# Kernel optimization log

Hardware: AMD Instinct MI355X
Metric: run time of the kernel (lower is better)

Reference implementation:

```python
import jax, jax.numpy as jnp
import numpy as np

# ---- static config (matches init_kwargs) ----
B, SX, SY, SZ = 1, 64, 64, 64
W = 32            # HIDDEN_DIM
L = 4             # num_fourier_layers
M1 = M2 = M3 = 8  # fourier modes per axis
PX = PY = PZ = 8  # domain padding
ALPHA = 0.05      # leaky relu slope
OUTC = 6


def conv3d(x, w, pad):
    # x: (B,C,D,H,W), w: (O,I,kd,kh,kw)
    return jax.lax.conv_general_dilated(
        x, w, window_strides=(1, 1, 1), padding=[(pad, pad)] * 3,
        dimension_numbers=('NCDHW', 'OIDHW', 'NCDHW'))


def pad1(x):
    # periodic=(0,0,0) -> zero pad 1 on every spatial side (matches ZeroPad3d chain)
    return jnp.pad(x, ((0, 0), (0, 0), (1, 1), (1, 1), (1, 1)))


def basic_block(x, w1, w2):
    # BasicBlock3D_Periodic with use_shortcut=False
    out = jax.nn.leaky_relu(conv3d(pad1(x), w1, 0), ALPHA)
    return conv3d(pad1(out), w2, 0)


def spec_apply(xft_slice, w):
    # xft_slice: complex (B,C,d1,d2,d3); w: (2C,2C,5,5,5)
    re_im = jnp.concatenate([xft_slice.real, xft_slice.imag], axis=1)  # (B,2C,...)
    out = conv3d(re_im, w, 2)                                          # (B,2C,...)
    b, c2, d1, d2, d3 = out.shape
    out = out.reshape(b, c2 // 2, 2, d1, d2, d3)
    return jax.lax.complex(out[:, :, 0], out[:, :, 1])


def spectral_conv(x, ws):
    # ws: (8, 2W, 2W, 5, 5, 5); mode-limited per-octant conv in frequency space
    b, c, n, m, l = x.shape
    xft = jnp.fft.rfftn(x, axes=(-3, -2, -1))  # (b,c,n,m,l//2+1) complex
    out = jnp.zeros((b, c, n, m, l // 2 + 1), dtype=xft.dtype)
    octs = [
        (slice(None, M1),  slice(None, M2)),
        (slice(n - M1, None), slice(None, M2)),
        (slice(None, M1),  slice(m - M2, None)),
        (slice(n - M1, None), slice(m - M2, None)),
        (slice(M1, n - M1), slice(None, M2)),
        (slice(None, M1),  slice(M2, m - M2)),
        (slice(M1, n - M1), slice(m - M2, None)),
        (slice(n - M1, None), slice(M2, m - M2)),
    ]
    for i, (s1, s2) in enumerate(octs):
        out = out.at[:, :, s1, s2, :M3].set(spec_apply(xft[:, :, s1, s2, :M3], ws[i]))
    return jnp.fft.irfftn(out, s=(n, m, l), axes=(-3, -2, -1))


def setup_inputs() -> dict:
    key = jax.random.key(0)
    ks = jax.random.split(key, 16)
    f32 = jnp.float32
    d = {
        'yeex': jax.random.normal(ks[0], (B, SX, SY, SZ), f32),
        'yeey': jax.random.normal(ks[1], (B, SX, SY, SZ), f32),
        'yeez': jax.random.normal(ks[2], (B, SX, SY, SZ), f32),
        'fc0_w': jax.random.normal(ks[3], (6, W), f32) * 0.1,
        'fc0_b': jax.random.normal(ks[4], (W,), f32) * 0.01,
        'spec_w': jax.random.normal(ks[5], (L, 8, 2 * W, 2 * W, 5, 5, 5), f32) * 0.02,
        'blk_w1': jax.random.normal(ks[6], (L, W, W, 3, 3, 3), f32) * 0.05,
        'blk_w2': jax.random.normal(ks[7], (L, W, W, 3, 3, 3), f32) * 0.05,
        'fc1_w': jax.random.normal(ks[8], (W, 128), f32) * 0.05,
        'fc1_b': jax.random.normal(ks[9], (128,), f32) * 0.01,
        'fc2_w': jax.random.normal(ks[10], (128, OUTC), f32) * 0.05,
        'fc2_b': jax.random.normal(ks[11], (OUTC,), f32) * 0.01,
    }
    return d


def reference(yeex, yeey, yeez, fc0_w, fc0_b, spec_w, blk_w1, blk_w2,
              fc1_w, fc1_b, fc2_w, fc2_b):
    b, sx, sy, sz = yeez.shape
    # normalized coordinate grid (3 channels), as in standard FNO get_grid
    gx = jnp.broadcast_to(jnp.linspace(0., 1., sx, dtype=yeex.dtype)[None, :, None, None], (b, sx, sy, sz))
    gy = jnp.broadcast_to(jnp.linspace(0., 1., sy, dtype=yeex.dtype)[None, None, :, None], (b, sx, sy, sz))
    gz = jnp.broadcast_to(jnp.linspace(0., 1., sz, dtype=yeex.dtype)[None, None, None, :], (b, sx, sy, sz))
    inp = jnp.stack([yeex, yeey, yeez, gx, gy, gz], axis=-1)  # (b,sx,sy,sz,6)

    x = inp @ fc0_w + fc0_b                      # lift: (b,sx,sy,sz,W)
    x = jnp.transpose(x, (0, 4, 1, 2, 3))        # (b,W,sx,sy,sz)
    x = jnp.pad(x, ((0, 0), (0, 0), (0, PX), (0, PY), (0, PZ)))

    for i in range(L):
        x1 = spectral_conv(x, spec_w[i])
        x2 = basic_block(x, blk_w1[i], blk_w2[i])
        x = x1 + x2 + x
        if i < L - 1:
            x = jax.nn.leaky_relu(x, ALPHA)

    x = x[:, :, :sx, :sy, :sz]                   # crop domain padding
    x = jnp.transpose(x, (0, 2, 3, 4, 1))        # (b,sx,sy,sz,W)
    x = jax.nn.leaky_relu(x @ fc1_w + fc1_b, ALPHA)
    return x @ fc2_w + fc2_b                     # (b,sx,sy,sz,OUTC)
```

## Files before the change

### kernel.cpp

```cpp
#include <hip/hip_runtime.h>
#include <math.h>

#define NS 72
#define NS2 (NS*NS)
#define NS3 (NS*NS*NS)
#define MZ 8
#define LALPHA 0.05f
#define CSCALE (1.0f/256.0f)

typedef _Float16 f16x8 __attribute__((ext_vector_type(8)));
typedef _Float16 f16x4 __attribute__((ext_vector_type(4)));
typedef float f32x4 __attribute__((ext_vector_type(4)));

__device__ __forceinline__ float leakyf(float v){ return v > 0.f ? v : LALPHA*v; }

__constant__ int c_RX0[8] = {0,64,0,64, 8,0,8,64};
__constant__ int c_RNX[8] = {8,8,8,8, 56,8,56,8};
__constant__ int c_RY0[8] = {0,0,64,64, 0,8,64,8};
__constant__ int c_RNY[8] = {8,8,8,8, 8,56,8,56};
__constant__ int c_Bbase[8] = {0,1728,3456,5184, 6912,15552,24192,32832};
__constant__ int c_BY[8]    = {12,12,12,12, 12,60,12,60};

__global__ void k_tw(float2* tw){
  int t = threadIdx.x;
  if (t < NS){
    double th = (2.0*M_PI/72.0)*(double)t;
    tw[t] = make_float2((float)cos(th), (float)sin(th));
  }
}

__global__ void k_wpackT(const float* __restrict__ w1, float* __restrict__ w1t){
  int e = blockIdx.x*256 + threadIdx.x;
  int j = e >> 5, c = e & 31;
  w1t[e] = w1[c*128 + j];
}

__global__ void k_fc0(const float* __restrict__ yx, const float* __restrict__ yy,
                      const float* __restrict__ yz, const float* __restrict__ w,
                      const float* __restrict__ b, float* __restrict__ X){
  int idx = blockIdx.x*256 + threadIdx.x;
  int z = idx % NS; int t = idx / NS; int y = t % NS; t /= NS; int x = t % NS; int c = t / NS;
  float v = 0.f;
  if (x < 64 && y < 64 && z < 64){
    int p = (x*64 + y)*64 + z;
    float i0 = yx[p], i1 = yy[p], i2 = yz[p];
    float gx = (float)x*(1.f/63.f), gy = (float)y*(1.f/63.f), gz = (float)z*(1.f/63.f);
    v = b[c] + i0*w[0*32+c] + i1*w[1*32+c] + i2*w[2*32+c]
             + gx*w[3*32+c] + gy*w[4*32+c] + gz*w[5*32+c];
  }
  X[idx] = v;
}

__global__ void k_zdft(const float* __restrict__ X, float2* __restrict__ A, const float2* __restrict__ tw){
  __shared__ float2 stw[NS];
  int tid = threadIdx.x;
  if (tid < NS) stw[tid] = tw[tid];
  __syncthreads();
  int f = blockIdx.x*256 + tid;
  const float* row = X + (size_t)f*NS;
  float ar[MZ], ai[MZ]; int tk[MZ];
  #pragma unroll
  for (int k=0;k<MZ;k++){ ar[k]=0.f; ai[k]=0.f; tk[k]=0; }
  for (int z4=0; z4<NS; z4+=4){
    float4 v4 = *(const float4*)(row + z4);
    float vs[4] = {v4.x, v4.y, v4.z, v4.w};
    #pragma unroll
    for (int zz=0; zz<4; zz++){
      float v = vs[zz];
      #pragma unroll
      for (int k=0;k<MZ;k++){
        float2 w = stw[tk[k]];
        ar[k] += v*w.x;
        ai[k] -= v*w.y;
        tk[k] += k; if (tk[k] >= NS) tk[k] -= NS;
      }
    }
  }
  float2* o = A + (size_t)f*MZ;
  #pragma unroll
  for (int k=0;k<MZ;k++) o[k] = make_float2(ar[k], ai[k]);
}

__global__ void k_ydft(const float2* __restrict__ A, float2* __restrict__ B, const float2* __restrict__ tw){
  __shared__ float2 stw[NS];
  int tid = threadIdx.x;
  if (tid < NS) stw[tid] = tw[tid];
  __syncthreads();
  int f = blockIdx.x*256 + tid;
  int ky = f % NS; int cx = f / NS;
  const float2* in = A + (size_t)cx*NS*MZ;
  float ar[MZ], ai[MZ];
  #pragma unroll
  for (int k=0;k<MZ;k++){ ar[k]=0.f; ai[k]=0.f; }
  int t = 0;
  for (int y=0;y<NS;y++){
    float2 w = stw[t]; t += ky; if (t>=NS) t-=NS;
    const float2* iy = in + y*MZ;
    #pragma unroll
    for (int k=0;k<MZ;k++){
      float2 v = iy[k];
      ar[k] += v.x*w.x + v.y*w.y;
      ai[k] += v.y*w.x - v.x*w.y;
    }
  }
  float2* o = B + (size_t)f*MZ;
  #pragma unroll
  for (int k=0;k<MZ;k++) o[k] = make_float2(ar[k], ai[k]);
}

__global__ void k_xdftL(const float2* __restrict__ B, float2* __restrict__ C, const float2* __restrict__ tw){
  __shared__ float2 stw[NS];
  int tid = threadIdx.x;
  if (tid < NS) stw[tid] = tw[tid];
  __syncthreads();
  int t = blockIdx.x*256 + tid;
  int h = t & 1; int t2 = t >> 1;
  int c = t2 >> 11; int l = t2 & 2047;
  int kx, ky;
  if (l < 576){ ky = l & 7; kx = l >> 3; }
  else if (l < 1152){ int e = l - 576; ky = 64 + (e & 7); kx = e >> 3; }
  else { int e = l - 1152; int kyi = e >> 4; int kxi = e & 15;
         ky = 8 + kyi; kx = (kxi < 8) ? kxi : 56 + kxi; }
  int k0 = h*4;
  const float2* in = B + ((size_t)c*NS2 + ky)*MZ + k0;
  float ar[4], ai[4];
  #pragma unroll
  for (int k=0;k<4;k++){ ar[k]=0.f; ai[k]=0.f; }
  int tt = 0;
  for (int x=0;x<NS;x++){
    float2 w = stw[tt]; tt += kx; if (tt>=NS) tt-=NS;
    const float2* ix = in + (size_t)x*NS*MZ;
    #pragma unroll
    for (int k=0;k<4;k++){
      float2 v = ix[k];
      ar[k] += v.x*w.x + v.y*w.y;
      ai[k] += v.y*w.x - v.x*w.y;
    }
  }
  float2* o = C + (((size_t)c*NS + kx)*NS + ky)*MZ + k0;
  #pragma unroll
  for (int k=0;k<4;k++) o[k] = make_float2(ar[k], ai[k]);
}

__global__ void k_wpackh(const float* __restrict__ W, _Float16* __restrict__ Ah){
  int e = blockIdx.x*256 + threadIdx.x;
  int i = e & 63; int o = (e>>6) & 63;
  int t2 = e >> 12; int tap = t2 % 125; int r = t2 / 125;
  const float* wr = W + (size_t)r*64*64*125;
  Ah[e] = (_Float16)wr[((size_t)(o*64 + (i&1)*32 + (i>>1)))*125 + tap];
}

__global__ void k_cpackh(const float2* __restrict__ C, _Float16* __restrict__ Bg){
  int g = blockIdx.x*256 + threadIdx.x;
  int ci = g & 31; int elem = g >> 5;
  int r = 0;
  #pragma unroll
  for (int k=1;k<8;k++) if (elem >= c_Bbase[k]) r = k;
  int el = elem - c_Bbase[r];
  int BY = c_BY[r];
  int q3 = el % 12; int tt = el / 12; int q2 = tt % BY; int q1 = tt / BY;
  int kxr = q1-2, kyr = q2-2, kzr = q3-2;
  float2 v = make_float2(0.f,0.f);
  if ((unsigned)kxr < (unsigned)c_RNX[r] && (unsigned)kyr < (unsigned)c_RNY[r] && (unsigned)kzr < 8u){
    v = C[(((size_t)ci*NS + (c_RX0[r]+kxr))*NS + (c_RY0[r]+kyr))*MZ + kzr];
  }
  _Float16* o = Bg + (size_t)elem*64 + 2*ci;
  o[0] = (_Float16)(v.x*CSCALE);
  o[1] = (_Float16)(v.y*CSCALE);
}

__global__ __launch_bounds__(64) void k_freqmfma(const _Float16* __restrict__ Ah,
                                                 const _Float16* __restrict__ Bg,
                                                 float* __restrict__ Pp){
  int gb = blockIdx.x;
  int ks = gb >> 8; int b = gb & 255;
  int r, til;
  if (b < 32){ r = b>>3; til = b&7; }
  else       { r = 4 + (b-32)/56; til = (b-32)%56; }
  int BY = c_BY[r];
  int q1, q2base;
  if (r==5 || r==7){ q1 = 2 + til/7; q2base = 2 + (til%7)*8; }
  else             { q1 = 2 + til;   q2base = 2; }
  int lane = threadIdx.x;
  int l15 = lane & 15, kg = lane >> 4;
  int q2l = q2base + (l15>>3), q3l = 2 + (l15&7);
  const _Float16* Ar = Ah + (size_t)r*125*4096;
  const _Float16* Br = Bg + (size_t)c_Bbase[r]*64;
  int lb = q2l*12 + q3l;
  f32x4 acc[4][4];
  f32x4 zz = {0.f,0.f,0.f,0.f};
  #pragma unroll
  for (int m=0;m<4;m++)
    #pragma unroll
    for (int n=0;n<4;n++) acc[m][n] = zz;
  int t0 = ks*16;
  int t1 = t0+16 < 125 ? t0+16 : 125;
  for (int tt=t0; tt<t1; tt++){
    int td = tt/25; int rm = tt - td*25; int th = rm/5; int tz = rm - th*5;
    const _Float16* At = Ar + tt*4096;
    f16x8 a[4][2];
    #pragma unroll
    for (int mt=0;mt<4;mt++){
      a[mt][0] = *(const f16x8*)(At + (mt*16+l15)*64 + kg*8);
      a[mt][1] = *(const f16x8*)(At + (mt*16+l15)*64 + 32 + kg*8);
    }
    int ebase = (q1 + td - 2)*BY*12 + lb + (th-2)*12 + (tz-2);
    f16x8 bf[4][2];
    #pragma unroll
    for (int nt=0;nt<4;nt++){
      const _Float16* bp = Br + (size_t)(ebase + nt*24)*64 + kg*8;
      bf[nt][0] = *(const f16x8*)(bp);
      bf[nt][1] = *(const f16x8*)(bp + 32);
    }
    #pragma unroll
    for (int mt=0;mt<4;mt++)
      #pragma unroll
      for (int nt=0;nt<4;nt++){
        acc[mt][nt] = __builtin_amdgcn_mfma_f32_16x16x32_f16(a[mt][0], bf[nt][0], acc[mt][nt],0,0,0);
        acc[mt][nt] = __builtin_amdgcn_mfma_f32_16x16x32_f16(a[mt][1], bf[nt][1], acc[mt][nt],0,0,0);
      }
  }
  float* base = Pp + (((size_t)ks*256 + b)*64 + lane)*64;
  #pragma unroll
  for (int mt=0;mt<4;mt++)
    #pragma unroll
    for (int nt=0;nt<4;nt++)
      *(f32x4*)(base + mt*16 + nt*4) = acc[mt][nt];
}

__global__ void k_fred(const float* __restrict__ Pp, float* __restrict__ Df){
  int t = blockIdx.x*256 + threadIdx.x;
  int mtnt = t & 15; int lane = (t>>4) & 63; int b = t >> 10;
  int mt = mtnt >> 2, nt = mtnt & 3;
  int r, til;
  if (b < 32){ r = b>>3; til = b&7; }
  else       { r = 4 + (b-32)/56; til = (b-32)%56; }
  int x0 = c_RX0[r], y0 = c_RY0[r];
  int q1, q2base;
  if (r==5 || r==7){ q1 = 2 + til/7; q2base = 2 + (til%7)*8; }
  else             { q1 = 2 + til;   q2base = 2; }
  int l15 = lane & 15, kg = lane >> 4;
  int q2l = q2base + (l15>>3), q3l = 2 + (l15&7);
  f32x4 s = {0.f,0.f,0.f,0.f};
  #pragma unroll
  for (int ks=0;ks<8;ks++){
    s += *(const f32x4*)(Pp + (((size_t)ks*256 + b)*64 + lane)*64 + mtnt*4);
  }
  int kx = x0 + q1 - 2;
  int kz = q3l - 2;
  int ky = y0 + q2l + nt*2 - 2;
  #pragma unroll
  for (int rg=0;rg<4;rg++){
    int o = mt*16 + kg*4 + rg;
    int co = o >> 1, reim = o & 1;
    Df[((((size_t)co*NS + kx)*NS + ky)*MZ + kz)*2 + reim] = s[rg]*256.0f;
  }
}

__global__ void k_invx(const float2* __restrict__ D, float2* __restrict__ E, const float2* __restrict__ tw){
  __shared__ float2 stw[NS];
  int tid = threadIdx.x;
  if (tid < NS) stw[tid] = tw[tid];
  __syncthreads();
  int f = blockIdx.x*256 + tid;
  int ky = f / 2304; int rem = f - ky*2304;
  int c = rem / NS; int x = rem - c*NS;
  const float2* in = D + ((size_t)c*NS2 + ky)*MZ;
  float ar[MZ], ai[MZ];
  #pragma unroll
  for (int k=0;k<MZ;k++){ ar[k]=0.f; ai[k]=0.f; }
  if (ky >= 8 && ky < 64){
    int t = 0;
    for (int kx=0;kx<8;kx++){
      float2 w = stw[t]; t += x; if (t>=NS) t-=NS;
      const float2* ix = in + (size_t)kx*NS*MZ;
      #pragma unroll
      for (int k=0;k<MZ;k++){
        float2 v = ix[k];
        ar[k] += v.x*w.x - v.y*w.y;
        ai[k] += v.x*w.y + v.y*w.x;
      }
    }
    t = (64*x) % NS;
    for (int kx=64;kx<NS;kx++){
      float2 w = stw[t]; t += x; if (t>=NS) t-=NS;
      const float2* ix = in + (size_t)kx*NS*MZ;
      #pragma unroll
      for (int k=0;k<MZ;k++){
        float2 v = ix[k];
        ar[k] += v.x*w.x - v.y*w.y;
        ai[k] += v.x*w.y + v.y*w.x;
      }
    }
  } else {
    int t = 0;
    for (int kx=0;kx<NS;kx++){
      float2 w = stw[t]; t += x; if (t>=NS) t-=NS;
      const float2* ix = in + (size_t)kx*NS*MZ;
      #pragma unroll
      for (int k=0;k<MZ;k++){
        float2 v = ix[k];
        ar[k] += v.x*w.x - v.y*w.y;
        ai[k] += v.x*w.y + v.y*w.x;
      }
    }
  }
  float2* o = E + (((size_t)c*NS + x)*NS + ky)*MZ;
  #pragma unroll
  for (int k=0;k<MZ;k++) o[k] = make_float2(ar[k]*(1.f/72.f), ai[k]*(1.f/72.f));
}

__global__ void k_invyz(const float2* __restrict__ E, _Float16* __restrict__ X1h, const float2* __restrict__ tw){
  __shared__ float2 stw[NS];
  int tid = threadIdx.x;
  if (tid < NS) stw[tid] = tw[tid];
  __syncthreads();
  int f = blockIdx.x*256 + tid;
  int y = f % NS; int t2 = f / NS; int x = t2 % NS; int c = t2 / NS;
  const float2* in = E + ((size_t)c*NS + x)*NS*MZ;
  float ar[MZ], ai[MZ];
  #pragma unroll
  for (int k=0;k<MZ;k++){ ar[k]=0.f; ai[k]=0.f; }
  int t = 0;
  for (int ky=0;ky<NS;ky++){
    float2 w = stw[t]; t += y; if (t>=NS) t-=NS;
    const float2* ik = in + ky*MZ;
    #pragma unroll
    for (int k=0;k<MZ;k++){
      float2 v = ik[k];
      ar[k] += v.x*w.x - v.y*w.y;
      ai[k] += v.x*w.y + v.y*w.x;
    }
  }
  const float scale = 1.f/(72.f*72.f);
  _Float16* o = X1h + (size_t)f*NS;
  int tk[MZ];
  #pragma unroll
  for (int k=0;k<MZ;k++) tk[k]=0;
  for (int z4=0; z4<NS; z4+=4){
    f16x4 hv;
    #pragma unroll
    for (int zz=0; zz<4; zz++){
      float acc = ar[0];
      #pragma unroll
      for (int k=1;k<MZ;k++){
        float2 w = stw[tk[k]];
        acc += 2.f*(ar[k]*w.x - ai[k]*w.y);
        tk[k] += k; if (tk[k] >= NS) tk[k] -= NS;
      }
      hv[zz] = (_Float16)(acc*scale);
    }
    *(f16x4*)(o + z4) = hv;
  }
}


__global__ void k_wcvt2(const float* __restrict__ w1, const float* __restrict__ w2,
                        _Float16* __restrict__ WhA, _Float16* __restrict__ WhB){
  int e = blockIdx.x*256 + threadIdx.x;
  int h = e >= 27648; int e2 = e - (h ? 27648 : 0);
  int tap = e2 >> 10; int co = (e2>>5)&31; int ci = e2&31;
  const float* w = h ? w2 : w1;
  _Float16* o = h ? WhB : WhA;
  o[e2] = (_Float16)w[(co*32+ci)*27 + tap];
}

__global__ void k_cvt16(const float* __restrict__ Xf, _Float16* __restrict__ Xg){
  int b = blockIdx.x;
  int tid = threadIdx.x;
  if (b >= 1458){
    _Float16* g = (b==1458) ? (Xg - 4096) : (Xg + (size_t)NS3*32);
    f16x8 zz = {0,0,0,0,0,0,0,0};
    f16x8* gp = (f16x8*)g;
    gp[tid] = zz; gp[tid+256] = zz;
    return;
  }
  int p = b*256 + tid;
  f16x8 o0,o1,o2,o3;
  #pragma unroll
  for (int c=0;c<8;c++){
    o0[c] = (_Float16)Xf[(size_t)c*NS3 + p];
    o1[c] = (_Float16)Xf[(size_t)(c+8)*NS3 + p];
    o2[c] = (_Float16)Xf[(size_t)(c+16)*NS3 + p];
    o3[c] = (_Float16)Xf[(size_t)(c+24)*NS3 + p];
  }
  f16x8* op = (f16x8*)(Xg + (size_t)p*32);
  op[0]=o0; op[1]=o1; op[2]=o2; op[3]=o3;
}

__global__ void k_zgH(_Float16* __restrict__ Hg){
  int e = blockIdx.x*256 + threadIdx.x;
  _Float16* g = (e < 512) ? (Hg - 4096 + e*8)
                          : (Hg + (size_t)NS3*32 + (size_t)(e-512)*8);
  f16x8 zz = {0,0,0,0,0,0,0,0};
  *(f16x8*)g = zz;
}

__global__ __launch_bounds__(192) void k_convm(const _Float16* __restrict__ Xg,
    const _Float16* __restrict__ Wh, float* __restrict__ OUT, _Float16* __restrict__ OUTH,
    const _Float16* __restrict__ X1h, const _Float16* __restrict__ XresH,
    int mode2, int do_leaky){
  __shared__ _Float16 sB[338*32];
  int tid = threadIdx.x;
  int orig = blockIdx.x;
  int xcd = orig & 7, loc = orig >> 3;
  int wg = xcd*243 + loc;
  int slab = wg/27, tb = wg - slab*27;
  int q0 = tb*192;
  int wid = tid >> 6;
  int lane = tid & 63;
  int l15 = lane & 15, kg = lane >> 4;
  f32x4 acc[2][4];
  f32x4 zz = {0.f,0.f,0.f,0.f};
  #pragma unroll
  for (int a=0;a<2;a++)
    #pragma unroll
    for (int b=0;b<4;b++) acc[a][b] = zz;
  int wbase = l15*32 + kg*8;
  int lbase = wid*64 + 73 + l15;
  for (int dx=0; dx<3; dx++){
    int xx = slab + dx - 1;
    if ((unsigned)xx >= 72u) continue;
    __syncthreads();
    {
      const f16x8* src = (const f16x8*)(Xg + ((long long)xx*5184 + q0 - 73)*32);
      f16x8* dst = (f16x8*)sB;
      for (int e=tid; e<1352; e+=192){
        int es = (e & ~3) | ((e & 3) ^ ((e >> 3) & 3));
        dst[es] = src[e];
      }
    }
    __syncthreads();
    const _Float16* Wdx = Wh + dx*9216;
    #pragma unroll
    for (int t9=0; t9<9; t9++){
      int off = ((t9/3)-1)*72 + (t9%3) - 1;
      const _Float16* wp = Wdx + t9*1024 + wbase;
      f16x8 a0 = *(const f16x8*)(wp);
      f16x8 a1 = *(const f16x8*)(wp + 512);
      int rr = lbase + off;
      const _Float16* bb = sB + (((rr << 2) | (kg ^ ((rr >> 1) & 3)))*8);
      f16x8 b0 = *(const f16x8*)(bb);
      f16x8 b1 = *(const f16x8*)(bb + 512);
      f16x8 b2 = *(const f16x8*)(bb + 1024);
      f16x8 b3 = *(const f16x8*)(bb + 1536);
      acc[0][0] = __builtin_amdgcn_mfma_f32_16x16x32_f16(a0,b0,acc[0][0],0,0,0);
      acc[0][1] = __builtin_amdgcn_mfma_f32_16x16x32_f16(a0,b1,acc[0][1],0,0,0);
      acc[0][2] = __builtin_amdgcn_mfma_f32_16x16x32_f16(a0,b2,acc[0][2],0,0,0);
      acc[0][3] = __builtin_amdgcn_mfma_f32_16x16x32_f16(a0,b3,acc[0][3],0,0,0);
      acc[1][0] = __builtin_amdgcn_mfma_f32_16x16x32_f16(a1,b0,acc[1][0],0,0,0);
      acc[1][1] = __builtin_amdgcn_mfma_f32_16x16x32_f16(a1,b1,acc[1][1],0,0,0);
      acc[1][2] = __builtin_amdgcn_mfma_f32_16x16x32_f16(a1,b2,acc[1][2],0,0,0);
      acc[1][3] = __builtin_amdgcn_mfma_f32_16x16x32_f16(a1,b3,acc[1][3],0,0,0);
    }
  }
  int q0w = q0 + wid*64;
  if (mode2){
    #pragma unroll
    for (int nt=0; nt<4; nt++){
      int q = q0w + nt*16 + l15;
      int y = q/72, z = q - y*72;
      bool edge = (y==0)||(y==71)||(z==0)||(z==71);
      #pragma unroll
      for (int c2=0;c2<2;c2++){
        #pragma unroll
        for (int r=0;r<4;r++){
          int co = c2*16 + kg*4 + r;
          size_t idx = (size_t)co*NS3 + (size_t)slab*5184 + q;
          float v = acc[c2][nt][r];
          if (!edge){
            v += (float)X1h[idx] + (float)XresH[((size_t)slab*5184 + q)*32 + co];
            if (do_leaky) v = leakyf(v);
          }
          OUT[idx] = v;
        }
      }
    }
  } else {
    #pragma unroll
    for (int nt=0; nt<4; nt++){
      int q = q0w + nt*16 + l15;
      int y = q/72, z = q - y*72;
      bool edge = (y==0)||(y==71)||(z==0)||(z==71);
      _Float16* hp = OUTH + ((size_t)slab*5184 + q)*32 + kg*4;
      #pragma unroll
      for (int c2=0;c2<2;c2++){
        f32x4 av = acc[c2][nt];
        f16x4 hv;
        #pragma unroll
        for (int r=0;r<4;r++){
          float v = av[r];
          if (!edge) v = leakyf(v);
          hv[r] = (_Float16)v;
        }
        *(f16x4*)(hp + c2*16) = hv;
      }
    }
  }
}

__global__ void k_corrH(_Float16* __restrict__ H, const _Float16* __restrict__ Xg,
                        const _Float16* __restrict__ Wh){
  int t = blockIdx.x*256 + threadIdx.x;
  int co = t & 31; int t2 = t >> 5;
  int e = t2 % 284; int x = t2 / 284;
  int y, z;
  if (e < 72){ y = 0; z = e; }
  else if (e < 144){ y = 71; z = e - 72; }
  else if (e < 214){ z = 0; y = e - 143; }
  else { z = 71; y = e - 213; }
  int q = y*72 + z;
  float corr = 0.f;
  for (int tap=0; tap<27; tap++){
    int dx = tap/9, rr = tap%9, dy = rr/3, dz = rr%3;
    int xx = x + dx - 1;
    if ((unsigned)xx >= 72u) continue;
    int yy = y + dy - 1, zz = z + dz - 1;
    if ((unsigned)yy < 72u && (unsigned)zz < 72u) continue;
    int lin = (xx*5184 + q + (dy-1)*72 + (dz-1))*32;
    const _Float16* V = Xg + lin;
    const _Float16* Wr = Wh + (tap*32 + co)*32;
    float s = 0.f;
    #pragma unroll
    for (int ci=0; ci<32; ci++) s += (float)V[ci]*(float)Wr[ci];
    corr += s;
  }
  size_t idx = ((size_t)x*5184 + q)*32 + co;
  float v = (float)H[idx] - corr;
  v = leakyf(v);
  H[idx] = (_Float16)v;
}

__global__ void k_corr(float* __restrict__ OUT, const _Float16* __restrict__ Xg,
                       const _Float16* __restrict__ Wh, const _Float16* __restrict__ X1h,
                       const _Float16* __restrict__ XresH, int mode2, int do_leaky){
  int t = blockIdx.x*256 + threadIdx.x;
  int co = t & 31; int t2 = t >> 5;
  int e = t2 % 284; int x = t2 / 284;
  int y, z;
  if (e < 72){ y = 0; z = e; }
  else if (e < 144){ y = 71; z = e - 72; }
  else if (e < 214){ z = 0; y = e - 143; }
  else { z = 71; y = e - 213; }
  int q = y*72 + z;
  float corr = 0.f;
  for (int tap=0; tap<27; tap++){
    int dx = tap/9, rr = tap%9, dy = rr/3, dz = rr%3;
    int xx = x + dx - 1;
    if ((unsigned)xx >= 72u) continue;
    int yy = y + dy - 1, zz = z + dz - 1;
    if ((unsigned)yy < 72u && (unsigned)zz < 72u) continue;
    int lin = (xx*5184 + q + (dy-1)*72 + (dz-1))*32;
    const _Float16* V = Xg + lin;
    const _Float16* Wr = Wh + (tap*32 + co)*32;
    float s = 0.f;
    #pragma unroll
    for (int ci=0; ci<32; ci++) s += (float)V[ci]*(float)Wr[ci];
    corr += s;
  }
  size_t idx = (size_t)co*NS3 + (size_t)x*5184 + q;
  float v = OUT[idx] - corr;
  if (mode2) v += (float)X1h[idx] + (float)XresH[((size_t)x*5184 + q)*32 + co];
  if (do_leaky) v = leakyf(v);
  OUT[idx] = v;
}

__global__ void k_head(const float* __restrict__ X, const float* __restrict__ w1t, const float* __restrict__ b1,
                       const float* __restrict__ w2, const float* __restrict__ b2, float* __restrict__ out){
  int tid = threadIdx.x;
  int p0 = blockIdx.x*256 + tid;
  float xin[2][32];
  float acc[2][6];
  float bb2[6];
  #pragma unroll
  for (int o=0;o<6;o++) bb2[o] = b2[o];
  #pragma unroll
  for (int vv=0; vv<2; vv++){
    int p = p0 + vv*131072;
    int z = p % 64; int t = p / 64; int y = t % 64; int x = t / 64;
    size_t q = ((size_t)x*NS + y)*NS + z;
    #pragma unroll
    for (int c=0;c<32;c++) xin[vv][c] = X[(size_t)c*NS3 + q];
    #pragma unroll
    for (int o=0;o<6;o++) acc[vv][o]=bb2[o];
  }
  for (int j=0;j<128;j++){
    const float4* wj = (const float4*)(w1t + j*32);
    float h0 = b1[j], h1 = h0;
    #pragma unroll
    for (int c4=0;c4<8;c4++){
      float4 w = wj[c4];
      h0 += xin[0][c4*4+0]*w.x + xin[0][c4*4+1]*w.y + xin[0][c4*4+2]*w.z + xin[0][c4*4+3]*w.w;
      h1 += xin[1][c4*4+0]*w.x + xin[1][c4*4+1]*w.y + xin[1][c4*4+2]*w.z + xin[1][c4*4+3]*w.w;
    }
    h0 = leakyf(h0); h1 = leakyf(h1);
    const float* s2j = w2 + j*6;
    #pragma unroll
    for (int o=0;o<6;o++){
      float wv = s2j[o];
      acc[0][o] += h0*wv;
      acc[1][o] += h1*wv;
    }
  }
  #pragma unroll
  for (int vv=0; vv<2; vv++){
    float* O = out + (size_t)(p0 + vv*131072)*6;
    #pragma unroll
    for (int o=0;o<6;o++) O[o]=acc[vv][o];
  }
}

extern "C" void kernel_launch(void* const* d_in, const int* in_sizes, int n_in,
                              void* d_out, int out_size, void* d_ws, size_t ws_size,
                              hipStream_t stream) {
  const float* yeex = (const float*)d_in[0];
  const float* yeey = (const float*)d_in[1];
  const float* yeez = (const float*)d_in[2];
  const float* fc0w = (const float*)d_in[3];
  const float* fc0b = (const float*)d_in[4];
  const float* specw= (const float*)d_in[5];
  const float* bw1  = (const float*)d_in[6];
  const float* bw2  = (const float*)d_in[7];
  const float* fc1w = (const float*)d_in[8];
  const float* fc1b = (const float*)d_in[9];
  const float* fc2w = (const float*)d_in[10];
  const float* fc2b = (const float*)d_in[11];
  float* out = (float*)d_out;
  float* ws  = (float*)d_ws;

  float*  P0 = ws;
  float*  X1s = ws + 11943936;
  float*  P2 = ws + 23887872;
  float2* A  = (float2*)(ws + 35831808);
  float2* B  = (float2*)(ws + 41140224);
  float2* Cf = (float2*)(ws + 46448640);
  float2* Df = (float2*)(ws + 51757056);
  float2* TW = (float2*)(ws + 57065472);
  float*  W1T = ws + 57065728;
  _Float16* Ah = (_Float16*)A;
  _Float16* Bg = (_Float16*)B;
  float*    Pp = X1s;
  _Float16* X1h = (_Float16*)X1s;
  _Float16* XhG = (_Float16*)(ws + 35831808) + 4096;
  _Float16* HhG = (_Float16*)(ws + 41807872) + 4096;
  _Float16* WhA = (_Float16*)(ws + 47783936);
  _Float16* WhB = (_Float16*)(ws + 47797760);

  float* curX = P0; float* curY = P2;

  k_tw<<<1,128,0,stream>>>(TW);
  k_wpackT<<<16,256,0,stream>>>(fc1w, W1T);
  k_fc0<<<46656,256,0,stream>>>(yeex,yeey,yeez,fc0w,fc0b,curX);
  for (int i=0;i<4;i++){
    k_zdft<<<648,256,0,stream>>>(curX, A, TW);
    k_ydft<<<648,256,0,stream>>>(A, B, TW);
    k_xdftL<<<512,256,0,stream>>>(B, Cf, TW);
    k_wpackh<<<16000,256,0,stream>>>(specw + (size_t)i*8*64*64*125, Ah);
    k_cpackh<<<5184,256,0,stream>>>(Cf, Bg);
    hipMemsetAsync(Df, 0, (size_t)1327104*8, stream);
    k_freqmfma<<<2048,64,0,stream>>>(Ah, Bg, Pp);
    k_fred<<<1024,256,0,stream>>>(Pp, (float*)Df);
    k_invx<<<648,256,0,stream>>>(Df, A, TW);
    k_invyz<<<648,256,0,stream>>>(A, X1h, TW);
    k_wcvt2<<<216,256,0,stream>>>(bw1 + (size_t)i*27648, bw2 + (size_t)i*27648, WhA, WhB);
    k_cvt16<<<1460,256,0,stream>>>(curX, XhG);
    k_zgH<<<4,256,0,stream>>>(HhG);
    k_convm<<<1944,192,0,stream>>>(XhG, WhA, nullptr, HhG, nullptr, nullptr, 0, 1);
    k_corrH<<<2556,256,0,stream>>>(HhG, XhG, WhA);
    k_convm<<<1944,192,0,stream>>>(HhG, WhB, curY, nullptr, X1h, XhG, 1, (i<3)?1:0);
    k_corr<<<2556,256,0,stream>>>(curY, HhG, WhB, X1h, XhG, 1, (i<3)?1:0);
    float* tmp = curX; curX = curY; curY = tmp;
  }
  k_head<<<512,256,0,stream>>>(curX, W1T, fc1b, fc2w, fc2b, out);
}
```

Baseline: 2.154 ms.

## Fuse split-K frequency MFMA and reduction into one block with LDS reduce

The split-K spectral MFMA kernel previously wrote eight partial tiles to global memory, and a separate kernel summed them and scattered the result into Df. Now one 512-thread block per tile runs the eight K-slices as eight wavefronts, reduces them in shared memory in four serialized phases, and writes Df directly. This removes the partial-sum global round trip and one launch. The cost is fewer, larger blocks (256 instead of 2048) and a serialized LDS reduction with barriers. The block index is also remapped to interleave tiles.

After: 2.117 ms. No clear change (-1.7%).

```diff
diff --git a/kernel.cpp b/kernel.cpp
--- a/kernel.cpp
+++ b/kernel.cpp
@@ -169,19 +169,22 @@
   o[1] = (_Float16)(v.y*CSCALE);
 }
 
-__global__ __launch_bounds__(64) void k_freqmfma(const _Float16* __restrict__ Ah,
-                                                 const _Float16* __restrict__ Bg,
-                                                 float* __restrict__ Pp){
-  int gb = blockIdx.x;
-  int ks = gb >> 8; int b = gb & 255;
+__global__ __launch_bounds__(512) void k_freqmfma2(const _Float16* __restrict__ Ah,
+                                                   const _Float16* __restrict__ Bg,
+                                                   float* __restrict__ Df){
+  __shared__ float sAcc[2][64*65];
+  int tid = threadIdx.x;
+  int orig = blockIdx.x;
+  int b = (orig & 7)*32 + (orig >> 3);
   int r, til;
   if (b < 32){ r = b>>3; til = b&7; }
   else       { r = 4 + (b-32)/56; til = (b-32)%56; }
-  int BY = c_BY[r];
+  int x0 = c_RX0[r], y0 = c_RY0[r], BY = c_BY[r];
   int q1, q2base;
   if (r==5 || r==7){ q1 = 2 + til/7; q2base = 2 + (til%7)*8; }
   else             { q1 = 2 + til;   q2base = 2; }
-  int lane = threadIdx.x;
+  int wv = tid >> 6;
+  int lane = tid & 63;
   int l15 = lane & 15, kg = lane >> 4;
   int q2l = q2base + (l15>>3), q3l = 2 + (l15&7);
   const _Float16* Ar = Ah + (size_t)r*125*4096;
@@ -193,7 +196,7 @@
   for (int m=0;m<4;m++)
     #pragma unroll
     for (int n=0;n<4;n++) acc[m][n] = zz;
-  int t0 = ks*16;
+  int t0 = wv*16;
   int t1 = t0+16 < 125 ? t0+16 : 125;
   for (int tt=t0; tt<t1; tt++){
     int td = tt/25; int rm = tt - td*25; int th = rm/5; int tz = rm - th*5;
@@ -220,40 +223,46 @@
         acc[mt][nt] = __builtin_amdgcn_mfma_f32_16x16x32_f16(a[mt][1], bf[nt][1], acc[mt][nt],0,0,0);
       }
   }
-  float* base = Pp + (((size_t)ks*256 + b)*64 + lane)*64;
-  #pragma unroll
-  for (int mt=0;mt<4;mt++)
-    #pragma unroll
-    for (int nt=0;nt<4;nt++)
-      *(f32x4*)(base + mt*16 + nt*4) = acc[mt][nt];
-}
-
-__global__ void k_fred(const float* __restrict__ Pp, float* __restrict__ Df){
-  int t = blockIdx.x*256 + threadIdx.x;
-  int mtnt = t & 15; int lane = (t>>4) & 63; int b = t >> 10;
-  int mt = mtnt >> 2, nt = mtnt & 3;
-  int r, til;
-  if (b < 32){ r = b>>3; til = b&7; }
-  else       { r = 4 + (b-32)/56; til = (b-32)%56; }
-  int x0 = c_RX0[r], y0 = c_RY0[r];
-  int q1, q2base;
-  if (r==5 || r==7){ q1 = 2 + til/7; q2base = 2 + (til%7)*8; }
-  else             { q1 = 2 + til;   q2base = 2; }
-  int l15 = lane & 15, kg = lane >> 4;
-  int q2l = q2base + (l15>>3), q3l = 2 + (l15&7);
-  f32x4 s = {0.f,0.f,0.f,0.f};
-  #pragma unroll
-  for (int ks=0;ks<8;ks++){
-    s += *(const f32x4*)(Pp + (((size_t)ks*256 + b)*64 + lane)*64 + mtnt*4);
-  }
+  int hb = wv >> 2, ph = wv & 3;
+  float* dst = sAcc[hb] + lane*65;
+  for (int p=0; p<4; p++){
+    if (ph == p){
+      #pragma unroll
+      for (int mt=0;mt<4;mt++)
+        #pragma unroll
+        for (int nt=0;nt<4;nt++){
+          int e = mt*16 + nt*4;
+          if (p == 0){
+            dst[e+0] = acc[mt][nt][0]; dst[e+1] = acc[mt][nt][1];
+            dst[e+2] = acc[mt][nt][2]; dst[e+3] = acc[mt][nt][3];
+          } else {
+            dst[e+0] += acc[mt][nt][0]; dst[e+1] += acc[mt][nt][1];
+            dst[e+2] += acc[mt][nt][2]; dst[e+3] += acc[mt][nt][3];
+          }
+        }
+    }
+    __syncthreads();
+  }
+  int lane2 = tid & 63;
+  int pr = tid >> 6;
+  int mt = pr >> 1, ntb = (pr & 1)*2;
+  int l15b = lane2 & 15, kgb = lane2 >> 4;
+  int q2b = q2base + (l15b>>3), q3b = 2 + (l15b&7);
   int kx = x0 + q1 - 2;
-  int kz = q3l - 2;
-  int ky = y0 + q2l + nt*2 - 2;
-  #pragma unroll
-  for (int rg=0;rg<4;rg++){
-    int o = mt*16 + kg*4 + rg;
-    int co = o >> 1, reim = o & 1;
-    Df[((((size_t)co*NS + kx)*NS + ky)*MZ + kz)*2 + reim] = s[rg]*256.0f;
+  int kz = q3b - 2;
+  const float* s0 = sAcc[0] + lane2*65;
+  const float* s1 = sAcc[1] + lane2*65;
+  #pragma unroll
+  for (int dn=0; dn<2; dn++){
+    int nt = ntb + dn;
+    int ky = y0 + q2b + nt*2 - 2;
+    #pragma unroll
+    for (int rg=0; rg<4; rg++){
+      int e = mt*16 + nt*4 + rg;
+      int o = mt*16 + kgb*4 + rg;
+      int co = o >> 1, reim = o & 1;
+      Df[((((size_t)co*NS + kx)*NS + ky)*MZ + kz)*2 + reim] = (s0[e] + s1[e])*256.0f;
+    }
   }
 }
 
@@ -639,7 +648,6 @@
   float*  W1T = ws + 57065728;
   _Float16* Ah = (_Float16*)A;
   _Float16* Bg = (_Float16*)B;
-  float*    Pp = X1s;
   _Float16* X1h = (_Float16*)X1s;
   _Float16* XhG = (_Float16*)(ws + 35831808) + 4096;
   _Float16* HhG = (_Float16*)(ws + 41807872) + 4096;
@@ -658,8 +666,7 @@
     k_wpackh<<<16000,256,0,stream>>>(specw + (size_t)i*8*64*64*125, Ah);
     k_cpackh<<<5184,256,0,stream>>>(Cf, Bg);
     hipMemsetAsync(Df, 0, (size_t)1327104*8, stream);
-    k_freqmfma<<<2048,64,0,stream>>>(Ah, Bg, Pp);
-    k_fred<<<1024,256,0,stream>>>(Pp, (float*)Df);
+    k_freqmfma2<<<256,512,0,stream>>>(Ah, Bg, (float*)Df);
     k_invx<<<648,256,0,stream>>>(Df, A, TW);
     k_invyz<<<648,256,0,stream>>>(A, X1h, TW);
     k_wcvt2<<<216,256,0,stream>>>(bw1 + (size_t)i*27648, bw2 + (size_t)i*27648, WhA, WhB);
```
